# Performance work log

Measured on AMD Instinct MI355X. Metric: run time of the kernel, lower is better.

Reference implementation:

```python
import jax, jax.numpy as jnp
import numpy as np

NOT_EPSILON = 1.0
B, K, Q, T = 2, 512, 512, 128


def swishmax(x, axis):
    # x * exp(x - max) normalized by sum(|.|) + 1 along `axis`
    xexp = x * jnp.exp(x - jnp.max(x, axis=axis, keepdims=True))
    return xexp / (jnp.sum(jnp.abs(xexp), axis=axis, keepdims=True) + NOT_EPSILON)


def setup_inputs() -> dict:
    key = jax.random.key(0)
    ks = jax.random.split(key, 8)
    scale = 1.0 / np.sqrt(T)
    return {
        "query_tokens": jax.random.normal(ks[0], (B, Q, T), dtype=jnp.float32),
        "key_tokens": jax.random.normal(ks[1], (B, K, T), dtype=jnp.float32),
        "value_tokens": jax.random.normal(ks[2], (B, K, T), dtype=jnp.float32),
        "Wk": jax.random.normal(ks[3], (T, T), dtype=jnp.float32) * scale,
        "Wq": jax.random.normal(ks[4], (T, T), dtype=jnp.float32) * scale,
        "Wv": jax.random.normal(ks[5], (T, T), dtype=jnp.float32) * scale,
        "Wl": jax.random.normal(ks[6], (T, T), dtype=jnp.float32) * scale,
        "Wo": jax.random.normal(ks[7], (T, T), dtype=jnp.float32) * scale,
    }


def reference(query_tokens, key_tokens, value_tokens, Wk, Wq, Wv, Wl, Wo):
    lin = lambda x, W: jnp.einsum('...t,ut->...u', x, W)  # nn.Linear(bias=False): x @ W.T
    k = lin(key_tokens, Wk)       # [B, K, T]
    q = lin(query_tokens, Wq)     # [B, Q, T]
    # outer-product broadcast over tokens: [B, K, Q, T]
    attention_raw = k[..., :, None, :] * q[..., None, :, :]
    attention_logits = lin(attention_raw, Wl)            # [B, K, Q, T]
    attention_scale = swishmax(attention_logits, axis=-2)  # normalize over Q (dim=-2)
    v = lin(value_tokens, Wv)     # [B, K, T]
    values_scaled = v[..., :, None, :] * attention_scale  # [B, K, Q, T]
    value_sum = values_scaled.sum(axis=-3)                # sum over K -> [B, Q, T]
    return lin(value_sum, Wo)
```

## Files before the change

kernel.cpp:

```cpp
#include <hip/hip_runtime.h>


using f16    = _Float16;
using f16x8  = __attribute__((ext_vector_type(8)))  f16;
using f32x16 = __attribute__((ext_vector_type(16))) float;

#define LOG2E 1.4426950408889634f

__device__ __forceinline__ float exp2_fast(float x) {
  float r;
  asm("v_exp_f32 %0, %1" : "=v"(r) : "v"(x));
  return r;
}

__device__ __forceinline__ f16x8 cvt8(float4 a, float4 b) {
  f16x8 r;
  r[0]=(f16)a.x; r[1]=(f16)a.y; r[2]=(f16)a.z; r[3]=(f16)a.w;
  r[4]=(f16)b.x; r[5]=(f16)b.y; r[6]=(f16)b.z; r[7]=(f16)b.w;
  return r;
}

__global__ __launch_bounds__(256, 2) void k1_proj(
    const float* __restrict__ q_tok, const float* __restrict__ k_tok,
    const float* __restrict__ v_tok, const float* __restrict__ Wq,
    const float* __restrict__ Wk,    const float* __restrict__ Wv,
    f16* __restrict__ qh, float* __restrict__ kls, float* __restrict__ vf)
{
  const int gid    = blockIdx.x;
  const int tensor = gid >> 4;
  const int sub    = gid & 15;
  const int b      = sub >> 3;
  const int rt     = sub & 7;
  const float* X = tensor==0 ? q_tok : (tensor==1 ? k_tok : v_tok);
  const float* W = tensor==0 ? Wq    : (tensor==1 ? Wk    : Wv);

  const int tid = threadIdx.x;
  const int w = tid >> 6, lane = tid & 63;
  const int l31 = lane & 31, lhi = lane >> 5;
  const int rbase = rt*64 + (w>>1)*32;
  const int cbase = (w&1)*64;

  f32x16 C0, C1;
  #pragma unroll
  for (int i=0;i<16;++i){ C0[i]=0.f; C1[i]=0.f; }

  #pragma unroll
  for (int kc=0; kc<8; ++kc) {
    const float* ap = X + (size_t)(b*512 + rbase + l31)*128 + kc*16 + 8*lhi;
    f16x8 a = cvt8(*(const float4*)ap, *(const float4*)(ap+4));
    const float* bp0 = W + (size_t)(cbase + l31)*128 + kc*16 + 8*lhi;
    f16x8 b0 = cvt8(*(const float4*)bp0, *(const float4*)(bp0+4));
    C0 = __builtin_amdgcn_mfma_f32_32x32x16_f16(a, b0, C0, 0, 0, 0);
    const float* bp1 = bp0 + 32*128;
    f16x8 b1 = cvt8(*(const float4*)bp1, *(const float4*)(bp1+4));
    C1 = __builtin_amdgcn_mfma_f32_32x32x16_f16(a, b1, C1, 0, 0, 0);
  }

  #pragma unroll
  for (int us=0; us<2; ++us) {
    #pragma unroll
    for (int r=0; r<16; ++r) {
      const int row = rbase + (r&3) + 8*(r>>2) + 4*lhi;
      const int col = cbase + us*32 + l31;
      const float val = us ? C1[r] : C0[r];
      const size_t idx = (size_t)(b*512 + row)*128 + col;
      if (tensor==0)      qh[idx]  = (f16)val;
      else if (tensor==1) kls[idx] = val * LOG2E;
      else                vf[idx]  = val;
    }
  }
}

__global__ __launch_bounds__(512, 2) void k2_main(
    const f16* __restrict__ qh, const float* __restrict__ kls,
    const float* __restrict__ vf, const float* __restrict__ Wl,
    float* __restrict__ vsum)
{
  const int gid  = blockIdx.x;
  const int b    = gid >> 7;
  const int half = (gid >> 6) & 1;
  const int grp  = gid & 63;
  const int kk0  = grp * 8;

  const int tid = threadIdx.x;
  const int w = tid >> 6, lane = tid & 63;
  const int l31 = lane & 31, lhi = lane >> 5;
  const int ubase = half * 64;
  const int qbase = w * 64;

  __shared__ f16   Bl[64][136];
  __shared__ float redm[8][64];
  __shared__ float reds[8][64];

  f16x8 af[2][8];
  #pragma unroll
  for (int qs=0; qs<2; ++qs)
    #pragma unroll
    for (int kc=0; kc<8; ++kc)
      af[qs][kc] = *(const f16x8*)(qh + (size_t)(b*512 + qbase + qs*32 + l31)*128
                                      + kc*16 + 8*lhi);

  const int bu  = tid >> 3;
  const int btc = tid & 7;
  const float* wlr = Wl + (size_t)(ubase + bu)*128 + btc*16;
  const float4 wl0 = *(const float4*)(wlr);
  const float4 wl1 = *(const float4*)(wlr+4);
  const float4 wl2 = *(const float4*)(wlr+8);
  const float4 wl3 = *(const float4*)(wlr+12);

  f32x16 acc[2][2];
  #pragma unroll
  for (int i=0;i<16;++i){ acc[0][0][i]=0.f; acc[0][1][i]=0.f;
                          acc[1][0][i]=0.f; acc[1][1][i]=0.f; }

  for (int kki=0; kki<8; ++kki) {
    const int kk = kk0 + kki;
    __syncthreads();
    {
      const float* kp = kls + (size_t)(b*512 + kk)*128 + btc*16;
      const float4 k0 = *(const float4*)(kp);
      const float4 k1 = *(const float4*)(kp+4);
      const float4 k2 = *(const float4*)(kp+8);
      const float4 k3 = *(const float4*)(kp+12);
      f16x8 o0, o1;
      o0[0]=(f16)(wl0.x*k0.x); o0[1]=(f16)(wl0.y*k0.y);
      o0[2]=(f16)(wl0.z*k0.z); o0[3]=(f16)(wl0.w*k0.w);
      o0[4]=(f16)(wl1.x*k1.x); o0[5]=(f16)(wl1.y*k1.y);
      o0[6]=(f16)(wl1.z*k1.z); o0[7]=(f16)(wl1.w*k1.w);
      o1[0]=(f16)(wl2.x*k2.x); o1[1]=(f16)(wl2.y*k2.y);
      o1[2]=(f16)(wl2.z*k2.z); o1[3]=(f16)(wl2.w*k2.w);
      o1[4]=(f16)(wl3.x*k3.x); o1[5]=(f16)(wl3.y*k3.y);
      o1[6]=(f16)(wl3.z*k3.z); o1[7]=(f16)(wl3.w*k3.w);
      *(f16x8*)(&Bl[bu][btc*16])     = o0;
      *(f16x8*)(&Bl[bu][btc*16 + 8]) = o1;
    }
    __syncthreads();

    f32x16 C[2][2];
    #pragma unroll
    for (int i=0;i<16;++i){ C[0][0][i]=0.f; C[0][1][i]=0.f;
                            C[1][0][i]=0.f; C[1][1][i]=0.f; }
    #pragma unroll
    for (int kc=0; kc<8; ++kc) {
      #pragma unroll
      for (int us=0; us<2; ++us) {
        f16x8 bfr = *(const f16x8*)(&Bl[us*32 + l31][kc*16 + 8*lhi]);
        C[0][us] = __builtin_amdgcn_mfma_f32_32x32x16_f16(af[0][kc], bfr, C[0][us], 0,0,0);
        C[1][us] = __builtin_amdgcn_mfma_f32_32x32x16_f16(af[1][kc], bfr, C[1][us], 0,0,0);
      }
    }

    float mx0 = -3.4e38f, mx1 = -3.4e38f;
    #pragma unroll
    for (int qs=0; qs<2; ++qs)
      #pragma unroll
      for (int r=0; r<16; ++r) { mx0 = fmaxf(mx0, C[qs][0][r]);
                                 mx1 = fmaxf(mx1, C[qs][1][r]); }
    mx0 = fmaxf(mx0, __shfl_xor(mx0, 32));
    mx1 = fmaxf(mx1, __shfl_xor(mx1, 32));
    if (lane < 32) { redm[w][lane] = mx0; redm[w][32+lane] = mx1; }
    __syncthreads();
    float M0 = redm[0][l31], M1 = redm[0][32+l31];
    #pragma unroll
    for (int ww=1; ww<8; ++ww) { M0 = fmaxf(M0, redm[ww][l31]);
                                 M1 = fmaxf(M1, redm[ww][32+l31]); }

    float s0 = 0.f, s1 = 0.f;
    #pragma unroll
    for (int qs=0; qs<2; ++qs)
      #pragma unroll
      for (int r=0; r<16; ++r) {
        const float y0 = C[qs][0][r], y1 = C[qs][1][r];
        const float t0 = y0 * exp2_fast(y0 - M0);
        const float t1 = y1 * exp2_fast(y1 - M1);
        C[qs][0][r] = t0; C[qs][1][r] = t1;
        s0 += fabsf(t0);  s1 += fabsf(t1);
      }
    s0 += __shfl_xor(s0, 32);
    s1 += __shfl_xor(s1, 32);
    if (lane < 32) { reds[w][lane] = s0; reds[w][32+lane] = s1; }
    __syncthreads();
    float S0 = 0.f, S1 = 0.f;
    #pragma unroll
    for (int ww=0; ww<8; ++ww) { S0 += reds[ww][l31];
                                 S1 += reds[ww][32+l31]; }
    const float v0  = vf[(size_t)(b*512+kk)*128 + ubase + l31];
    const float v1  = vf[(size_t)(b*512+kk)*128 + ubase + 32 + l31];
    const float su0 = v0 / (S0 + LOG2E);
    const float su1 = v1 / (S1 + LOG2E);

    #pragma unroll
    for (int qs=0; qs<2; ++qs)
      #pragma unroll
      for (int r=0; r<16; ++r) {
        acc[qs][0][r] = fmaf(su0, C[qs][0][r], acc[qs][0][r]);
        acc[qs][1][r] = fmaf(su1, C[qs][1][r], acc[qs][1][r]);
      }
  }

  #pragma unroll
  for (int qs=0; qs<2; ++qs)
    #pragma unroll
    for (int us=0; us<2; ++us)
      #pragma unroll
      for (int r=0; r<16; ++r) {
        const int q  = qbase + qs*32 + (r&3) + 8*(r>>2) + 4*lhi;
        const int uu = ubase + us*32 + l31;
        atomicAdd(vsum + (size_t)(b*512 + q)*128 + uu, acc[qs][us][r]);
      }
}

__global__ __launch_bounds__(256, 2) void k3_out(
    const float* __restrict__ vsum, const float* __restrict__ Wo,
    float* __restrict__ out)
{
  const int sub = blockIdx.x;
  const int b = sub >> 3, rt = sub & 7;
  const int tid = threadIdx.x;
  const int w = tid >> 6, lane = tid & 63;
  const int l31 = lane & 31, lhi = lane >> 5;
  const int rbase = rt*64 + (w>>1)*32;
  const int cbase = (w&1)*64;

  f32x16 C0, C1;
  #pragma unroll
  for (int i=0;i<16;++i){ C0[i]=0.f; C1[i]=0.f; }

  #pragma unroll
  for (int kc=0; kc<8; ++kc) {
    const float* ap = vsum + (size_t)(b*512 + rbase + l31)*128 + kc*16 + 8*lhi;
    f16x8 a = cvt8(*(const float4*)ap, *(const float4*)(ap+4));
    const float* bp0 = Wo + (size_t)(cbase + l31)*128 + kc*16 + 8*lhi;
    f16x8 b0 = cvt8(*(const float4*)bp0, *(const float4*)(bp0+4));
    C0 = __builtin_amdgcn_mfma_f32_32x32x16_f16(a, b0, C0, 0, 0, 0);
    const float* bp1 = bp0 + 32*128;
    f16x8 b1 = cvt8(*(const float4*)bp1, *(const float4*)(bp1+4));
    C1 = __builtin_amdgcn_mfma_f32_32x32x16_f16(a, b1, C1, 0, 0, 0);
  }

  #pragma unroll
  for (int us=0; us<2; ++us)
    #pragma unroll
    for (int r=0; r<16; ++r) {
      const int row = rbase + (r&3) + 8*(r>>2) + 4*lhi;
      const int col = cbase + us*32 + l31;
      out[(size_t)(b*512 + row)*128 + col] = us ? C1[r] : C0[r];
    }
}

extern "C" void kernel_launch(void* const* d_in, const int* in_sizes, int n_in,
                              void* d_out, int out_size, void* d_ws, size_t ws_size,
                              hipStream_t stream) {
  const float* q_tok = (const float*)d_in[0];
  const float* k_tok = (const float*)d_in[1];
  const float* v_tok = (const float*)d_in[2];
  const float* Wk    = (const float*)d_in[3];
  const float* Wq    = (const float*)d_in[4];
  const float* Wv    = (const float*)d_in[5];
  const float* Wl    = (const float*)d_in[6];
  const float* Wo    = (const float*)d_in[7];

  char* ws = (char*)d_ws;
  f16*   qh   = (f16*)  (ws);
  float* kls  = (float*)(ws + 262144);
  float* vf   = (float*)(ws + 786432);
  float* vsum = (float*)(ws + 1310720);

  hipMemsetAsync(vsum, 0, 524288, stream);
  k1_proj<<<48, 256, 0, stream>>>(q_tok, k_tok, v_tok, Wq, Wk, Wv, qh, kls, vf);
  k2_main<<<256, 512, 0, stream>>>(qh, kls, vf, Wl, vsum);
  k3_out<<<16, 256, 0, stream>>>(vsum, Wo, (float*)d_out);
}
```

Measured before the change: 142.4 us.

## Single-pass unshifted swishmax, double-buffer Bl, fold vsum zeroing into projection kernel

The softmax-like normalization now computes y*exp2(y) without subtracting the max first. Max and abs-sum are reduced together in one shared-memory pass, and the +1 epsilon is rescaled by exp2(M), which removes one barrier and one reduction round per K step. The Bl tile is double-buffered, with next K rows prefetched into registers. A fragments are reloaded from global/L1 each step instead of held in registers, and the separate memset of vsum is folded into k1. The unshifted exp can overflow if logits grow large, and re-reading A from memory adds load traffic in exchange for fewer registers.

```diff
diff --git a/kernel.cpp b/kernel.cpp
--- a/kernel.cpp
+++ b/kernel.cpp
@@ -7,10 +7,8 @@
 
 #define LOG2E 1.4426950408889634f
 
-__device__ __forceinline__ float exp2_fast(float x) {
-  float r;
-  asm("v_exp_f32 %0, %1" : "=v"(r) : "v"(x));
-  return r;
+__device__ __forceinline__ float exp2b(float x) {
+  return __builtin_amdgcn_exp2f(x);
 }
 
 __device__ __forceinline__ f16x8 cvt8(float4 a, float4 b) {
@@ -24,8 +22,15 @@
     const float* __restrict__ q_tok, const float* __restrict__ k_tok,
     const float* __restrict__ v_tok, const float* __restrict__ Wq,
     const float* __restrict__ Wk,    const float* __restrict__ Wv,
-    f16* __restrict__ qh, float* __restrict__ kls, float* __restrict__ vf)
+    f16* __restrict__ qh, float* __restrict__ kls, float* __restrict__ vf,
+    float* __restrict__ vsum)
 {
+  {
+    const int idx = blockIdx.x*256 + threadIdx.x;
+    const float4 z = make_float4(0.f,0.f,0.f,0.f);
+    for (int j = idx; j < 32768; j += 48*256) ((float4*)vsum)[j] = z;
+  }
+
   const int gid    = blockIdx.x;
   const int tensor = gid >> 4;
   const int sub    = gid & 15;
@@ -88,17 +93,8 @@
   const int ubase = half * 64;
   const int qbase = w * 64;
 
-  __shared__ f16   Bl[64][136];
-  __shared__ float redm[8][64];
-  __shared__ float reds[8][64];
-
-  f16x8 af[2][8];
-  #pragma unroll
-  for (int qs=0; qs<2; ++qs)
-    #pragma unroll
-    for (int kc=0; kc<8; ++kc)
-      af[qs][kc] = *(const f16x8*)(qh + (size_t)(b*512 + qbase + qs*32 + l31)*128
-                                      + kc*16 + 8*lhi);
+  __shared__ f16    Bl[2][64][136];
+  __shared__ float2 red[2][8][64];
 
   const int bu  = tid >> 3;
   const int btc = tid & 7;
@@ -108,86 +104,104 @@
   const float4 wl2 = *(const float4*)(wlr+8);
   const float4 wl3 = *(const float4*)(wlr+12);
 
+  const float* kbase = kls + (size_t)(b*512 + kk0)*128 + btc*16;
+  const f16*   abase = qh  + (size_t)(b*512 + qbase + l31)*128 + 8*lhi;
+  const float* vbase = vf  + (size_t)(b*512 + kk0)*128 + ubase;
+
   f32x16 acc[2][2];
   #pragma unroll
   for (int i=0;i<16;++i){ acc[0][0][i]=0.f; acc[0][1][i]=0.f;
                           acc[1][0][i]=0.f; acc[1][1][i]=0.f; }
 
-  for (int kki=0; kki<8; ++kki) {
-    const int kk = kk0 + kki;
-    __syncthreads();
-    {
-      const float* kp = kls + (size_t)(b*512 + kk)*128 + btc*16;
-      const float4 k0 = *(const float4*)(kp);
-      const float4 k1 = *(const float4*)(kp+4);
-      const float4 k2 = *(const float4*)(kp+8);
-      const float4 k3 = *(const float4*)(kp+12);
-      f16x8 o0, o1;
-      o0[0]=(f16)(wl0.x*k0.x); o0[1]=(f16)(wl0.y*k0.y);
-      o0[2]=(f16)(wl0.z*k0.z); o0[3]=(f16)(wl0.w*k0.w);
-      o0[4]=(f16)(wl1.x*k1.x); o0[5]=(f16)(wl1.y*k1.y);
-      o0[6]=(f16)(wl1.z*k1.z); o0[7]=(f16)(wl1.w*k1.w);
-      o1[0]=(f16)(wl2.x*k2.x); o1[1]=(f16)(wl2.y*k2.y);
-      o1[2]=(f16)(wl2.z*k2.z); o1[3]=(f16)(wl2.w*k2.w);
-      o1[4]=(f16)(wl3.x*k3.x); o1[5]=(f16)(wl3.y*k3.y);
-      o1[6]=(f16)(wl3.z*k3.z); o1[7]=(f16)(wl3.w*k3.w);
-      *(f16x8*)(&Bl[bu][btc*16])     = o0;
-      *(f16x8*)(&Bl[bu][btc*16 + 8]) = o1;
-    }
-    __syncthreads();
+  {
+    const float4 k0 = *(const float4*)(kbase);
+    const float4 k1 = *(const float4*)(kbase+4);
+    const float4 k2 = *(const float4*)(kbase+8);
+    const float4 k3 = *(const float4*)(kbase+12);
+    float4 a0 = make_float4(wl0.x*k0.x, wl0.y*k0.y, wl0.z*k0.z, wl0.w*k0.w);
+    float4 a1 = make_float4(wl1.x*k1.x, wl1.y*k1.y, wl1.z*k1.z, wl1.w*k1.w);
+    float4 a2 = make_float4(wl2.x*k2.x, wl2.y*k2.y, wl2.z*k2.z, wl2.w*k2.w);
+    float4 a3 = make_float4(wl3.x*k3.x, wl3.y*k3.y, wl3.z*k3.z, wl3.w*k3.w);
+    *(f16x8*)(&Bl[0][bu][btc*16])     = cvt8(a0, a1);
+    *(f16x8*)(&Bl[0][bu][btc*16 + 8]) = cvt8(a2, a3);
+  }
+  float4 n0 = *(const float4*)(kbase+128);
+  float4 n1 = *(const float4*)(kbase+132);
+  float4 n2 = *(const float4*)(kbase+136);
+  float4 n3 = *(const float4*)(kbase+140);
+  __syncthreads();
+
+  for (int i=0; i<8; ++i) {
+    const int cur = i & 1;
+
+    const float v0 = vbase[i*128 + l31];
+    const float v1 = vbase[i*128 + 32 + l31];
+
+    if (i < 7) {
+      float4 a0 = make_float4(wl0.x*n0.x, wl0.y*n0.y, wl0.z*n0.z, wl0.w*n0.w);
+      float4 a1 = make_float4(wl1.x*n1.x, wl1.y*n1.y, wl1.z*n1.z, wl1.w*n1.w);
+      float4 a2 = make_float4(wl2.x*n2.x, wl2.y*n2.y, wl2.z*n2.z, wl2.w*n2.w);
+      float4 a3 = make_float4(wl3.x*n3.x, wl3.y*n3.y, wl3.z*n3.z, wl3.w*n3.w);
+      *(f16x8*)(&Bl[cur^1][bu][btc*16])     = cvt8(a0, a1);
+      *(f16x8*)(&Bl[cur^1][bu][btc*16 + 8]) = cvt8(a2, a3);
+      if (i < 6) {
+        const float* kp = kbase + (i+2)*128;
+        n0 = *(const float4*)(kp);   n1 = *(const float4*)(kp+4);
+        n2 = *(const float4*)(kp+8); n3 = *(const float4*)(kp+12);
+      }
+    }
 
     f32x16 C[2][2];
     #pragma unroll
-    for (int i=0;i<16;++i){ C[0][0][i]=0.f; C[0][1][i]=0.f;
-                            C[1][0][i]=0.f; C[1][1][i]=0.f; }
+    for (int j=0;j<16;++j){ C[0][0][j]=0.f; C[0][1][j]=0.f;
+                            C[1][0][j]=0.f; C[1][1][j]=0.f; }
     #pragma unroll
     for (int kc=0; kc<8; ++kc) {
+      f16x8 a0 = *(const f16x8*)(abase + kc*16);
+      f16x8 a1 = *(const f16x8*)(abase + 32*128 + kc*16);
       #pragma unroll
       for (int us=0; us<2; ++us) {
-        f16x8 bfr = *(const f16x8*)(&Bl[us*32 + l31][kc*16 + 8*lhi]);
-        C[0][us] = __builtin_amdgcn_mfma_f32_32x32x16_f16(af[0][kc], bfr, C[0][us], 0,0,0);
-        C[1][us] = __builtin_amdgcn_mfma_f32_32x32x16_f16(af[1][kc], bfr, C[1][us], 0,0,0);
-      }
-    }
-
-    float mx0 = -3.4e38f, mx1 = -3.4e38f;
+        f16x8 bfr = *(const f16x8*)(&Bl[cur][us*32 + l31][kc*16 + 8*lhi]);
+        C[0][us] = __builtin_amdgcn_mfma_f32_32x32x16_f16(a0, bfr, C[0][us], 0,0,0);
+        C[1][us] = __builtin_amdgcn_mfma_f32_32x32x16_f16(a1, bfr, C[1][us], 0,0,0);
+      }
+    }
+
+    float mx0a=-3.4e38f, mx0b=-3.4e38f, mx1a=-3.4e38f, mx1b=-3.4e38f;
+    float s0a=0.f, s0b=0.f, s1a=0.f, s1b=0.f;
     #pragma unroll
     for (int qs=0; qs<2; ++qs)
       #pragma unroll
-      for (int r=0; r<16; ++r) { mx0 = fmaxf(mx0, C[qs][0][r]);
-                                 mx1 = fmaxf(mx1, C[qs][1][r]); }
+      for (int r=0; r<16; ++r) {
+        const float y0 = C[qs][0][r], y1 = C[qs][1][r];
+        const float p0 = y0 * exp2b(y0);
+        const float p1 = y1 * exp2b(y1);
+        C[qs][0][r] = p0; C[qs][1][r] = p1;
+        if (r & 1) { mx0b=fmaxf(mx0b,y0); s0b+=fabsf(p0);
+                     mx1b=fmaxf(mx1b,y1); s1b+=fabsf(p1); }
+        else       { mx0a=fmaxf(mx0a,y0); s0a+=fabsf(p0);
+                     mx1a=fmaxf(mx1a,y1); s1a+=fabsf(p1); }
+      }
+    float mx0 = fmaxf(mx0a,mx0b), mx1 = fmaxf(mx1a,mx1b);
+    float sm0 = s0a+s0b,          sm1 = s1a+s1b;
     mx0 = fmaxf(mx0, __shfl_xor(mx0, 32));
     mx1 = fmaxf(mx1, __shfl_xor(mx1, 32));
-    if (lane < 32) { redm[w][lane] = mx0; redm[w][32+lane] = mx1; }
+    sm0 += __shfl_xor(sm0, 32);
+    sm1 += __shfl_xor(sm1, 32);
+    red[cur][w][lane] = lhi ? make_float2(mx1, sm1) : make_float2(mx0, sm0);
+
     __syncthreads();
-    float M0 = redm[0][l31], M1 = redm[0][32+l31];
-    #pragma unroll
-    for (int ww=1; ww<8; ++ww) { M0 = fmaxf(M0, redm[ww][l31]);
-                                 M1 = fmaxf(M1, redm[ww][32+l31]); }
-
-    float s0 = 0.f, s1 = 0.f;
-    #pragma unroll
-    for (int qs=0; qs<2; ++qs)
-      #pragma unroll
-      for (int r=0; r<16; ++r) {
-        const float y0 = C[qs][0][r], y1 = C[qs][1][r];
-        const float t0 = y0 * exp2_fast(y0 - M0);
-        const float t1 = y1 * exp2_fast(y1 - M1);
-        C[qs][0][r] = t0; C[qs][1][r] = t1;
-        s0 += fabsf(t0);  s1 += fabsf(t1);
-      }
-    s0 += __shfl_xor(s0, 32);
-    s1 += __shfl_xor(s1, 32);
-    if (lane < 32) { reds[w][lane] = s0; reds[w][32+lane] = s1; }
-    __syncthreads();
-    float S0 = 0.f, S1 = 0.f;
-    #pragma unroll
-    for (int ww=0; ww<8; ++ww) { S0 += reds[ww][l31];
-                                 S1 += reds[ww][32+l31]; }
-    const float v0  = vf[(size_t)(b*512+kk)*128 + ubase + l31];
-    const float v1  = vf[(size_t)(b*512+kk)*128 + ubase + 32 + l31];
-    const float su0 = v0 / (S0 + LOG2E);
-    const float su1 = v1 / (S1 + LOG2E);
+
+    float M0=-3.4e38f, S0=0.f, M1=-3.4e38f, S1=0.f;
+    #pragma unroll
+    for (int ww=0; ww<8; ++ww) {
+      const float2 t0 = red[cur][ww][l31];
+      const float2 t1 = red[cur][ww][32+l31];
+      M0 = fmaxf(M0, t0.x); S0 += t0.y;
+      M1 = fmaxf(M1, t1.x); S1 += t1.y;
+    }
+    const float su0 = v0 / (S0 + LOG2E * exp2b(M0));
+    const float su1 = v1 / (S1 + LOG2E * exp2b(M1));
 
     #pragma unroll
     for (int qs=0; qs<2; ++qs)
@@ -196,6 +210,8 @@
         acc[qs][0][r] = fmaf(su0, C[qs][0][r], acc[qs][0][r]);
         acc[qs][1][r] = fmaf(su1, C[qs][1][r], acc[qs][1][r]);
       }
+
+    __syncthreads();
   }
 
   #pragma unroll
@@ -266,8 +282,7 @@
   float* vf   = (float*)(ws + 786432);
   float* vsum = (float*)(ws + 1310720);
 
-  hipMemsetAsync(vsum, 0, 524288, stream);
-  k1_proj<<<48, 256, 0, stream>>>(q_tok, k_tok, v_tok, Wq, Wk, Wv, qh, kls, vf);
+  k1_proj<<<48, 256, 0, stream>>>(q_tok, k_tok, v_tok, Wq, Wk, Wv, qh, kls, vf, vsum);
   k2_main<<<256, 512, 0, stream>>>(qh, kls, vf, Wl, vsum);
   k3_out<<<16, 256, 0, stream>>>(vsum, Wo, (float*)d_out);
 }
```

New measurement: 141.9 us. About the same (-0.4%).
